# Optimization experiments

Measured on AMD Instinct MI355X. Metric: run time of the kernel, lower is better.

Reference implementation:

```python
import jax, jax.numpy as jnp
import numpy as np

# Insertion order of keys == output channel order (matches OrderedDict in torch module)
MAPPING = {
    "nodata": [0],
    "water": [1, 2, 3],
    "forest": [4, 5, 6, 7, 8, 9, 10, 11, 12, 13],
    "shrub": [14, 15, 16, 17, 18, 19],
    "grass": [20, 21, 22, 23, 24, 25, 26, 27],
    "crop": [28, 29, 30, 31, 32, 33, 34, 35, 36, 37],
    "urban": [38, 39, 40, 41, 42, 43, 44, 45],
    "bare": [46, 47, 48, 49, 50, 51],
    "wetland": [52, 53, 54, 55, 56],
    "snow": [57, 58],
    "moss": [59, 60, 61],
    "cloud": [62, 63],
}
B, C, H, W = 8, 64, 512, 512
K = len(MAPPING)
# static gather indices: flat channel index and its group id
_IDX = np.concatenate([np.asarray(v, dtype=np.int32) for v in MAPPING.values()])
_GID = np.concatenate([np.full(len(v), g, dtype=np.int32) for g, v in enumerate(MAPPING.values())])


def setup_inputs() -> dict:
    key = jax.random.key(0)
    pred_lr = jax.random.normal(key, (B, C, H, W), dtype=jnp.float32)
    # conv heads are mean-initialized: weight = 1/len(group), bias = 0
    weights = jnp.concatenate([
        jnp.full((len(v),), 1.0 / max(1, len(v)), dtype=jnp.float32)
        for v in MAPPING.values()
    ])  # [sum(len(group))] == [64]
    biases = jnp.zeros((K,), dtype=jnp.float32)
    return {"pred_lr": pred_lr, "weights": weights, "biases": biases}


def reference(pred_lr, weights, biases):
    # Equivalent to: for each group g, 1x1 conv over gathered channels pred_lr[:, idxs]
    # Expressed as one sparse (scattered) K x C mixing matrix -> single contraction.
    Wmat = jnp.zeros((K, C), dtype=weights.dtype).at[_GID, _IDX].set(weights)
    pred_hr = jnp.einsum('bchw,kc->bkhw', pred_lr, Wmat) + biases[None, :, None, None]
    return pred_hr  # [B, K, H, W]; class names = list(MAPPING.keys())
```

## Files before the change

kernel.cpp:

```cpp
#include <hip/hip_runtime.h>


#define NB 8
#define NC 64
#define NK 12
#define NP (512 * 512)
#define NPV (NP / 4)

__global__ __launch_bounds__(256) void
hier_invert_kernel(const float* __restrict__ in,
                   const float* __restrict__ w,
                   const float* __restrict__ bias,
                   float* __restrict__ out) {
    __shared__ float sw[NC];
    __shared__ float sb[NK];
    const int tid = threadIdx.x;
    if (tid < NC) sw[tid] = w[tid];
    if (tid < NK) sb[tid] = bias[tid];
    __syncthreads();

    const long long t = (long long)blockIdx.x * blockDim.x + tid;
    const int b = (int)(t >> 16);
    const int p = (int)(t & (NPV - 1));

    const float4* __restrict__ in4 =
        (const float4*)in + (long long)b * NC * NPV + p;
    float4* __restrict__ out4 =
        (float4*)out + (long long)b * NK * NPV + p;

    constexpr int gs[NK + 1] = {0, 1, 4, 14, 20, 28, 38, 46, 52, 57, 59, 62, 64};

#pragma unroll
    for (int k = 0; k < NK; ++k) {
        const float bk = sb[k];
        float4 acc = make_float4(bk, bk, bk, bk);
#pragma unroll
        for (int c = gs[k]; c < gs[k + 1]; ++c) {
            const float4 v = in4[(long long)c * NPV];
            const float wc = sw[c];
            acc.x += wc * v.x;
            acc.y += wc * v.y;
            acc.z += wc * v.z;
            acc.w += wc * v.w;
        }
        out4[(long long)k * NPV] = acc;
    }
}

extern "C" void kernel_launch(void* const* d_in, const int* in_sizes, int n_in,
                              void* d_out, int out_size, void* d_ws, size_t ws_size,
                              hipStream_t stream) {
    const float* in   = (const float*)d_in[0];
    const float* w    = (const float*)d_in[1];
    const float* bias = (const float*)d_in[2];
    float* out        = (float*)d_out;

    const int total_threads = NB * NPV;
    const int block = 256;
    const int grid = total_threads / block;
    hier_invert_kernel<<<grid, block, 0, stream>>>(in, w, bias, out);
}
```

Before: 699.0 us.

## Process two float4 per thread with nontemporal loads/stores and drop LDS staging

Each thread now handles two float4 pixel vectors, which halves the grid and doubles the memory requests in flight per thread. Loads and stores use nontemporal builtins so the streamed input and output do not pollute the caches. Weights and bias are read directly from global memory instead of being staged through shared memory, which removes the block-wide barrier. In exchange, register pressure rises and the grid has fewer waves to hide latency.

```diff
diff --git a/kernel.cpp b/kernel.cpp
--- a/kernel.cpp
+++ b/kernel.cpp
@@ -6,44 +6,45 @@
 #define NK 12
 #define NP (512 * 512)
 #define NPV (NP / 4)
+#define F4_PER_THREAD 2
+#define BLOCK 256
+#define TILE (BLOCK * F4_PER_THREAD)
+#define BLOCKS_PER_B (NPV / TILE)
 
-__global__ __launch_bounds__(256) void
+typedef float v4f __attribute__((ext_vector_type(4)));
+
+__global__ __launch_bounds__(BLOCK) void
 hier_invert_kernel(const float* __restrict__ in,
                    const float* __restrict__ w,
                    const float* __restrict__ bias,
                    float* __restrict__ out) {
-    __shared__ float sw[NC];
-    __shared__ float sb[NK];
     const int tid = threadIdx.x;
-    if (tid < NC) sw[tid] = w[tid];
-    if (tid < NK) sb[tid] = bias[tid];
-    __syncthreads();
+    const int b    = blockIdx.x >> 7;
+    const int pblk = (blockIdx.x & 127) << 9;
+    const int p = pblk + tid;
 
-    const long long t = (long long)blockIdx.x * blockDim.x + tid;
-    const int b = (int)(t >> 16);
-    const int p = (int)(t & (NPV - 1));
-
-    const float4* __restrict__ in4 =
-        (const float4*)in + (long long)b * NC * NPV + p;
-    float4* __restrict__ out4 =
-        (float4*)out + (long long)b * NK * NPV + p;
+    const v4f* __restrict__ in4 =
+        (const v4f*)in + (long long)b * NC * NPV + p;
+    v4f* __restrict__ out4 =
+        (v4f*)out + (long long)b * NK * NPV + p;
 
     constexpr int gs[NK + 1] = {0, 1, 4, 14, 20, 28, 38, 46, 52, 57, 59, 62, 64};
 
 #pragma unroll
     for (int k = 0; k < NK; ++k) {
-        const float bk = sb[k];
-        float4 acc = make_float4(bk, bk, bk, bk);
+        const float bk = bias[k];
+        v4f acc0 = {bk, bk, bk, bk};
+        v4f acc1 = acc0;
 #pragma unroll
         for (int c = gs[k]; c < gs[k + 1]; ++c) {
-            const float4 v = in4[(long long)c * NPV];
-            const float wc = sw[c];
-            acc.x += wc * v.x;
-            acc.y += wc * v.y;
-            acc.z += wc * v.z;
-            acc.w += wc * v.w;
+            const float wc = w[c];
+            const v4f v0 = __builtin_nontemporal_load(&in4[(long long)c * NPV]);
+            const v4f v1 = __builtin_nontemporal_load(&in4[(long long)c * NPV + BLOCK]);
+            acc0 += wc * v0;
+            acc1 += wc * v1;
         }
-        out4[(long long)k * NPV] = acc;
+        __builtin_nontemporal_store(acc0, &out4[(long long)k * NPV]);
+        __builtin_nontemporal_store(acc1, &out4[(long long)k * NPV + BLOCK]);
     }
 }
 
@@ -55,8 +56,6 @@
     const float* bias = (const float*)d_in[2];
     float* out        = (float*)d_out;
 
-    const int total_threads = NB * NPV;
-    const int block = 256;
-    const int grid = total_threads / block;
-    hier_invert_kernel<<<grid, block, 0, stream>>>(in, w, bias, out);
+    const int grid = NB * BLOCKS_PER_B;
+    hier_invert_kernel<<<grid, BLOCK, 0, stream>>>(in, w, bias, out);
 }
```

New measurement: 687.0 us. About the same (-1.7%).
